# Kernel optimization log

Hardware: AMD Instinct MI355X
Metric: run time of the kernel (lower is better)

The kernel has to match this reference:

```python
import jax, jax.numpy as jnp
import numpy as np

TEMP = 5.0  # temperature_init
# All C(4,2)=6 keep-2-of-4 patterns for 2:4 semi-structured sparsity
PATTERNS = jnp.array([[1,1,0,0],[1,0,1,0],[1,0,0,1],[0,1,1,0],[0,1,0,1],[0,0,1,1]], dtype=jnp.float32)


def masked_linear(x, w, b, alpha, ids):
    # x: [N, I], w: [O, I], alpha: [A, O, I//4, 6], ids: [N]
    A, O, G, P = alpha.shape
    probs = jax.nn.softmax(alpha / TEMP, axis=-1)            # [A, O, G, 6]
    mask = jnp.einsum('aogp,pk->aogk', probs, PATTERNS)      # [A, O, G, 4]
    wm = w[None, :, :] * mask.reshape(A, O, G * 4)           # [A, O, I] per-agent masked weight
    y = jnp.einsum('ni,aoi->nao', x, wm)                     # dense per-agent GEMM
    y = jnp.take_along_axis(y, ids[:, None, None], axis=1)[:, 0, :]
    return y + b


def gru_cell(x, h, w_ih, w_hh, b_ih, b_hh):
    gi = x @ w_ih.T + b_ih
    gh = h @ w_hh.T + b_hh
    i_r, i_z, i_n = jnp.split(gi, 3, axis=-1)
    h_r, h_z, h_n = jnp.split(gh, 3, axis=-1)
    r = jax.nn.sigmoid(i_r + h_r)
    z = jax.nn.sigmoid(i_z + h_z)
    n = jnp.tanh(i_n + r * h_n)
    return (1.0 - z) * n + z * h


def setup_inputs() -> dict:
    key = jax.random.key(0)
    ks = jax.random.split(key, 20)
    B, A, E, H, NA = 1024, 8, 64, 512, 16
    s = 0.05
    d = {}
    d['inputs'] = jax.random.normal(ks[0], (B, A, E), jnp.float32)
    d['hidden_state'] = jax.random.normal(ks[1], (B, A, H), jnp.float32)
    d['agent_ids'] = jax.random.randint(ks[2], (B, A), 0, A, jnp.int32)
    d['fc1_w'] = jax.random.normal(ks[3], (H, E), jnp.float32) * s
    d['fc1_b'] = jax.random.normal(ks[4], (H,), jnp.float32) * s
    d['fc1_alpha'] = jax.random.normal(ks[5], (A, H, E // 4, 6), jnp.float32)
    d['gru_w_ih'] = jax.random.normal(ks[6], (3 * H, H), jnp.float32) * s
    d['gru_w_hh'] = jax.random.normal(ks[7], (3 * H, H), jnp.float32) * s
    d['gru_b_ih'] = jax.random.normal(ks[8], (3 * H,), jnp.float32) * s
    d['gru_b_hh'] = jax.random.normal(ks[9], (3 * H,), jnp.float32) * s
    d['fc2_w'] = jax.random.normal(ks[10], (H, H), jnp.float32) * s
    d['fc2_b'] = jax.random.normal(ks[11], (H,), jnp.float32) * s
    d['fc2_alpha'] = jax.random.normal(ks[12], (A, H, H // 4, 6), jnp.float32)
    d['fc3_w'] = jax.random.normal(ks[13], (H, H), jnp.float32) * s
    d['fc3_b'] = jax.random.normal(ks[14], (H,), jnp.float32) * s
    d['fc3_alpha'] = jax.random.normal(ks[15], (A, H, H // 4, 6), jnp.float32)
    d['fc4_w'] = jax.random.normal(ks[16], (NA, H), jnp.float32) * s
    d['fc4_b'] = jax.random.normal(ks[17], (NA,), jnp.float32) * s
    d['fc4_alpha'] = jax.random.normal(ks[18], (A, NA, H // 4, 6), jnp.float32)
    return d


def reference(inputs, hidden_state, agent_ids,
              fc1_w, fc1_b, fc1_alpha,
              gru_w_ih, gru_w_hh, gru_b_ih, gru_b_hh,
              fc2_w, fc2_b, fc2_alpha,
              fc3_w, fc3_b, fc3_alpha,
              fc4_w, fc4_b, fc4_alpha):
    b, a, e = inputs.shape
    H = hidden_state.shape[-1]
    x = inputs.reshape(-1, e)
    ids = agent_ids.reshape(-1)
    x = jax.nn.relu(masked_linear(x, fc1_w, fc1_b, fc1_alpha, ids))
    h = gru_cell(x, hidden_state.reshape(-1, H), gru_w_ih, gru_w_hh, gru_b_ih, gru_b_hh)
    q = jax.nn.relu(masked_linear(h, fc2_w, fc2_b, fc2_alpha, ids))
    q = jax.nn.relu(masked_linear(q, fc3_w, fc3_b, fc3_alpha, ids))
    q = masked_linear(q, fc4_w, fc4_b, fc4_alpha, ids)
    return q.reshape(b, a, -1), h.reshape(b, a, -1)
```

## Files before the change

### kernel.cpp

```cpp
#include <hip/hip_runtime.h>
#include <hip/hip_bf16.h>

typedef unsigned short ushort_t;
typedef __bf16 bf16x8 __attribute__((ext_vector_type(8)));
typedef unsigned short us8 __attribute__((ext_vector_type(8)));
typedef float f32x4 __attribute__((ext_vector_type(4)));

__device__ __forceinline__ ushort_t f2b(float f) {
    union { float f; unsigned int u; } v; v.f = f;
    unsigned int u = v.u;
    unsigned int r = (u + 0x7FFFu + ((u >> 16) & 1u)) >> 16;
    return (ushort_t)r;
}
__device__ __forceinline__ float sigmoidf_(float x) {
    return 1.f / (1.f + __expf(-x));
}
__device__ __forceinline__ void store_o(ushort_t* p, float v) { *p = f2b(v); }
__device__ __forceinline__ void store_o(float* p, float v) { *p = v; }

__global__ void fill_kernel(float* out, long long n, float val) {
    long long i = (long long)blockIdx.x * blockDim.x + threadIdx.x;
    if (i < n) out[i] = val;
}

#define PACKSZ(O, K) ((long long)((O) >= 64 ? (O) >> 6 : 1) * ((K) >> 5) * 2048)

__global__ void sort_kernel(const int* __restrict__ ids, int N,
                            int* __restrict__ perm, int* __restrict__ seg,
                            int4* __restrict__ ttab, int* __restrict__ tcount) {
    __shared__ int hist[16][8];
    __shared__ int wbase[16][8];
    __shared__ int atot[8];
    __shared__ int abase[8];
    int tid = threadIdx.x, wave = tid >> 6, lane = tid & 63;
    int base = wave * 512;
    unsigned long long lt = (lane == 63) ? 0x7fffffffffffffffull
                                         : ((1ull << lane) - 1ull);
    int myid[8], rank[8];
    int run[8] = {0, 0, 0, 0, 0, 0, 0, 0};
    #pragma unroll
    for (int i = 0; i < 8; i++) myid[i] = ids[base + i * 64 + lane] & 7;
    #pragma unroll
    for (int i = 0; i < 8; i++) {
        int a = myid[i];
        int r = 0;
        #pragma unroll
        for (int a2 = 0; a2 < 8; a2++) {
            unsigned long long m = __ballot(a == a2);
            if (a2 == a) r = run[a2] + __popcll(m & lt);
            run[a2] += __popcll(m);
        }
        rank[i] = r;
    }
    if (lane == 0) {
        #pragma unroll
        for (int a = 0; a < 8; a++) hist[wave][a] = run[a];
    }
    __syncthreads();
    if (tid < 8) {
        int a = tid, s = 0;
        for (int w = 0; w < 16; w++) { wbase[w][a] = s; s += hist[w][a]; }
        atot[a] = s;
    }
    __syncthreads();
    if (tid == 0) {
        int s = 0;
        for (int a = 0; a < 8; a++) { abase[a] = s; seg[a] = s; s += atot[a]; }
        seg[8] = s;
        int T = 0;
        for (int a = 0; a < 8; a++)
            for (int m = abase[a]; m < abase[a] + atot[a]; m += 64) {
                int e = abase[a] + atot[a];
                if (e > m + 64) e = m + 64;
                ttab[T++] = make_int4(a, m, e, 0);
            }
        *tcount = T;
    }
    __syncthreads();
    #pragma unroll
    for (int i = 0; i < 8; i++) {
        int a = myid[i];
        perm[abase[a] + wbase[wave][a] + rank[i]] = base + i * 64 + lane;
    }
}

__device__ __forceinline__ void maskw_item(const float* __restrict__ alpha,
                                           const float* __restrict__ w,
                                           ushort_t* __restrict__ wm,
                                           long long idx, int O, int G, int dup) {
    int g = (int)(idx % G);
    long long t2 = idx / G;
    int o = (int)(t2 % O);
    int a = (int)(t2 / O);
    const float* al = alpha + idx * 6;
    float p[6];
    float mx = -1e30f;
    #pragma unroll
    for (int i = 0; i < 6; i++) { p[i] = al[i] * 0.2f; mx = fmaxf(mx, p[i]); }
    float s = 0.f;
    #pragma unroll
    for (int i = 0; i < 6; i++) { p[i] = __expf(p[i] - mx); s += p[i]; }
    float inv = 1.f / s;
    #pragma unroll
    for (int i = 0; i < 6; i++) p[i] *= inv;
    float mk[4] = { p[0] + p[1] + p[2], p[0] + p[3] + p[4],
                    p[1] + p[3] + p[5], p[2] + p[4] + p[5] };
    int K = G * 4;
    const float* wr = w + (long long)o * K + g * 4;
    ushort_t* base = wm + (long long)a * PACKSZ(O, K);
    int k0 = g * 4;
    int c = o >> 6, su = (o >> 4) & 3, n = o & 15;
    int kk = k0 >> 5, q = (k0 >> 3) & 3, e0 = k0 & 7;
    long long off = (((long long)(c * (K >> 5) + kk) * 4 + su) * 64 + (q * 16 + n)) * 8 + e0;
    #pragma unroll
    for (int t = 0; t < 4; t++) {
        ushort_t v = f2b(wr[t] * mk[t]);
        base[off + t] = v;
        if (dup) {
            base[off + t + 512] = v;
            base[off + t + 1024] = v;
            base[off + t + 1536] = v;
        }
    }
}

__device__ __forceinline__ void canon_gather_item(const float* __restrict__ src,
                                                  ushort_t* __restrict__ dst,
                                                  const int* __restrict__ perm,
                                                  int ld, long long i) {
    long long base = i * 8;
    int pos = (int)(base / ld);
    int k = (int)(base % ld);
    int row = perm[pos] & 8191;
    const float* s = src + (long long)row * ld + k;
    us8 v;
    #pragma unroll
    for (int e = 0; e < 8; e++) v[e] = f2b(s[e]);
    *(us8*)(dst + base) = v;
}

__device__ __forceinline__ void canon_pack_item(const float* __restrict__ src,
                                                ushort_t* __restrict__ dst,
                                                long long i) {
    long long base = i * 8;
    int o_full = (int)(base >> 9);
    int k0 = (int)(base & 511);
    int g = o_full >> 9, o = o_full & 511;
    int c = o >> 6, su = (o >> 4) & 3, n = o & 15;
    int kk = k0 >> 5, q = (k0 >> 3) & 3;
    long long off = (long long)g * 262144 +
        (((long long)(c * 16 + kk) * 4 + su) * 64 + (q * 16 + n)) * 8;
    us8 v;
    #pragma unroll
    for (int e = 0; e < 8; e++) v[e] = f2b(src[base + e]);
    *(us8*)(dst + off) = v;
}

#define PB0 256
#define PB1 2048
#define PB2 2048
#define PB3 64
#define PB4 256
#define PB5 2048
#define PB6 384
#define PB7 384
#define PREP_BLOCKS (PB0+PB1+PB2+PB3+PB4+PB5+PB6+PB7)

__global__ void prep_kernel(const float* fc1_al, const float* fc1_w, ushort_t* wm1,
                            const float* fc2_al, const float* fc2_w, ushort_t* wm2,
                            const float* fc3_al, const float* fc3_w, ushort_t* wm3,
                            const float* fc4_al, const float* fc4_w, ushort_t* wm4,
                            const float* inputs, ushort_t* inp_pos,
                            const float* hidden, ushort_t* hid_pos,
                            const float* wih, ushort_t* wihp,
                            const float* whh, ushort_t* whhp,
                            const int* perm) {
    int b = blockIdx.x;
    int tid = threadIdx.x;
    if (b < PB0) { maskw_item(fc1_al, fc1_w, wm1, (long long)b * 256 + tid, 512, 16, 0); return; }
    b -= PB0;
    if (b < PB1) { maskw_item(fc2_al, fc2_w, wm2, (long long)b * 256 + tid, 512, 128, 0); return; }
    b -= PB1;
    if (b < PB2) { maskw_item(fc3_al, fc3_w, wm3, (long long)b * 256 + tid, 512, 128, 0); return; }
    b -= PB2;
    if (b < PB3) { maskw_item(fc4_al, fc4_w, wm4, (long long)b * 256 + tid, 16, 128, 1); return; }
    b -= PB3;
    if (b < PB4) { canon_gather_item(inputs, inp_pos, perm, 64, (long long)b * 256 + tid); return; }
    b -= PB4;
    if (b < PB5) { canon_gather_item(hidden, hid_pos, perm, 512, (long long)b * 256 + tid); return; }
    b -= PB5;
    if (b < PB6) { canon_pack_item(wih, wihp, (long long)b * 256 + tid); return; }
    b -= PB6;
    canon_pack_item(whh, whhp, (long long)b * 256 + tid);
}

#define BM 64
#define BN 64

template <typename OT>
__launch_bounds__(256, 4)
__global__ void gemm_tiled(const ushort_t* __restrict__ In, int ldin,
                           const ushort_t* __restrict__ Wpk, long long wstride,
                           const float* __restrict__ bias,
                           OT* __restrict__ Out, int ldo,
                           const int4* __restrict__ ttab,
                           const int* __restrict__ tcount,
                           const int* __restrict__ scatter,
                           int O, int K, int relu) {
    int t = blockIdx.x;
    if (t >= *tcount) return;
    int4 tt = ttab[t];
    int a = tt.x, pos0 = tt.y, pos1 = tt.z;
    int o0 = blockIdx.y * BN;

    __shared__ ushort_t As[2][2048];

    int tid = threadIdx.x;
    int wave = tid >> 6, lane = tid & 63;
    int wr = (wave >> 1) & 1, wc = wave & 1;
    int quad = lane >> 4, l16 = lane & 15;
    int srow = tid >> 2, sgrp = tid & 3;
    int wsoff = (srow * 4 + (sgrp ^ ((srow >> 2) & 3))) * 8;
    int rl = (l16 * 4 + (quad ^ ((l16 >> 2) & 3))) * 8;

    int apos = pos0 + srow;
    int apos_c = apos < pos1 ? apos : (pos1 - 1);
    const ushort_t* aptr = In + (long long)apos_c * ldin + sgrp * 8;

    const ushort_t* wb = Wpk + (long long)a * wstride +
        (long long)blockIdx.y * (K >> 5) * 2048 + lane * 8;

    f32x4 acc[2][2];
    #pragma unroll
    for (int i = 0; i < 2; i++)
        #pragma unroll
        for (int j = 0; j < 2; j++) acc[i][j] = (f32x4){0.f, 0.f, 0.f, 0.f};

    int KKh = K >> 6;
    for (int k2 = 0; k2 < KKh; k2++) {
        int kk = k2 * 2;
        us8 av0 = *(const us8*)(aptr + kk * 32);
        us8 av1 = *(const us8*)(aptr + kk * 32 + 32);
        bf16x8 b00 = *(const bf16x8*)(wb + (kk * 4 + wc * 2 + 0) * 512);
        bf16x8 b01 = *(const bf16x8*)(wb + (kk * 4 + wc * 2 + 1) * 512);
        bf16x8 b10 = *(const bf16x8*)(wb + ((kk + 1) * 4 + wc * 2 + 0) * 512);
        bf16x8 b11 = *(const bf16x8*)(wb + ((kk + 1) * 4 + wc * 2 + 1) * 512);
        __syncthreads();
        *(us8*)(&As[0][wsoff]) = av0;
        *(us8*)(&As[1][wsoff]) = av1;
        __syncthreads();
        bf16x8 af0[2], af1[2];
        af0[0] = *(const bf16x8*)(&As[0][(wr * 2 + 0) * 512 + rl]);
        af0[1] = *(const bf16x8*)(&As[0][(wr * 2 + 1) * 512 + rl]);
        af1[0] = *(const bf16x8*)(&As[1][(wr * 2 + 0) * 512 + rl]);
        af1[1] = *(const bf16x8*)(&As[1][(wr * 2 + 1) * 512 + rl]);
        #pragma unroll
        for (int i = 0; i < 2; i++) {
            acc[i][0] = __builtin_amdgcn_mfma_f32_16x16x32_bf16(af0[i], b00, acc[i][0], 0, 0, 0);
            acc[i][1] = __builtin_amdgcn_mfma_f32_16x16x32_bf16(af0[i], b01, acc[i][1], 0, 0, 0);
        }
        #pragma unroll
        for (int i = 0; i < 2; i++) {
            acc[i][0] = __builtin_amdgcn_mfma_f32_16x16x32_bf16(af1[i], b10, acc[i][0], 0, 0, 0);
            acc[i][1] = __builtin_amdgcn_mfma_f32_16x16x32_bf16(af1[i], b11, acc[i][1], 0, 0, 0);
        }
    }

    #pragma unroll
    for (int i = 0; i < 2; i++) {
        int mbase = wr * 32 + i * 16 + quad * 4;
        #pragma unroll
        for (int j = 0; j < 2; j++) {
            int col = o0 + wc * 32 + j * 16 + l16;
            if (col < O) {
                float bias_v = bias ? bias[col] : 0.f;
                #pragma unroll
                for (int r = 0; r < 4; r++) {
                    int pos = pos0 + mbase + r;
                    if (pos < pos1) {
                        float v = acc[i][j][r] + bias_v;
                        if (relu) v = fmaxf(v, 0.f);
                        int orow = (scatter ? scatter[pos] : pos) & 8191;
                        store_o(&Out[(long long)orow * ldo + col], v);
                    }
                }
            }
        }
    }
}

__launch_bounds__(512, 2)
__global__ void gru_fused(const ushort_t* __restrict__ y1,
                          const ushort_t* __restrict__ hid_pos,
                          const float* __restrict__ hidden_f,
                          const ushort_t* __restrict__ wihp,
                          const ushort_t* __restrict__ whhp,
                          const float* __restrict__ bih,
                          const float* __restrict__ bhh,
                          const int* __restrict__ perm,
                          float* __restrict__ out_h_f,
                          ushort_t* __restrict__ hp,
                          int N, int H) {
    int m0 = blockIdx.x * 128;

    __shared__ ushort_t Ay[4096];
    __shared__ ushort_t Ah[4096];
    __shared__ ushort_t Bt[6][2048];

    int tid = threadIdx.x;
    int wave = tid >> 6, lane = tid & 63;
    int wr = wave >> 1, wc = wave & 1;
    int quad = lane >> 4, l16 = lane & 15;
    int srow = tid >> 2, sgrp = tid & 3;
    int wsoff = (srow * 4 + (sgrp ^ ((srow >> 2) & 3))) * 8;
    int rl = (l16 * 4 + (quad ^ ((l16 >> 2) & 3))) * 8;

    const ushort_t* ay_p = y1 + (long long)(m0 + srow) * H + sgrp * 8;
    const ushort_t* ah_p = hid_pos + (long long)(m0 + srow) * H + sgrp * 8;

    const ushort_t* wbs[3];
    int wg[3];
    #pragma unroll
    for (int q = 0; q < 3; q++) {
        int s = q * 512 + tid;
        int g = s >> 8, so = s & 255;
        wg[q] = s;
        wbs[q] = ((g < 3) ? (wihp + (long long)g * 262144)
                          : (whhp + (long long)(g - 3) * 262144)) +
                 (long long)blockIdx.y * 16 * 2048 + so * 8;
    }

    f32x4 acc[4][2][2];
    #pragma unroll
    for (int g = 0; g < 4; g++)
        #pragma unroll
        for (int i = 0; i < 2; i++)
            #pragma unroll
            for (int j = 0; j < 2; j++) acc[g][i][j] = (f32x4){0.f, 0.f, 0.f, 0.f};

    for (int kk = 0; kk < 16; kk++) {
        us8 va = *(const us8*)(ay_p + kk * 32);
        us8 vh = *(const us8*)(ah_p + kk * 32);
        us8 vb[3];
        #pragma unroll
        for (int q = 0; q < 3; q++) vb[q] = *(const us8*)(wbs[q] + kk * 2048);
        __syncthreads();
        *(us8*)(&Ay[wsoff]) = va;
        *(us8*)(&Ah[wsoff]) = vh;
        #pragma unroll
        for (int q = 0; q < 3; q++) {
            int s = wg[q];
            *(us8*)(&Bt[s >> 8][(s & 255) * 8]) = vb[q];
        }
        __syncthreads();

        bf16x8 ayf[2], ahf[2];
        #pragma unroll
        for (int u = 0; u < 2; u++) {
            ayf[u] = *(const bf16x8*)(&Ay[(wr * 2 + u) * 512 + rl]);
            ahf[u] = *(const bf16x8*)(&Ah[(wr * 2 + u) * 512 + rl]);
        }
        #pragma unroll
        for (int g = 0; g < 3; g++) {
            bf16x8 bw[2], bu[2];
            #pragma unroll
            for (int u = 0; u < 2; u++) {
                bw[u] = *(const bf16x8*)(&Bt[g][(wc * 2 + u) * 512 + lane * 8]);
                bu[u] = *(const bf16x8*)(&Bt[g + 3][(wc * 2 + u) * 512 + lane * 8]);
            }
            int ai = (g < 2) ? g : 2;
            int ah2 = (g < 2) ? g : 3;
            #pragma unroll
            for (int i = 0; i < 2; i++)
                #pragma unroll
                for (int j = 0; j < 2; j++) {
                    acc[ai][i][j] = __builtin_amdgcn_mfma_f32_16x16x32_bf16(
                        ayf[i], bw[j], acc[ai][i][j], 0, 0, 0);
                    acc[ah2][i][j] = __builtin_amdgcn_mfma_f32_16x16x32_bf16(
                        ahf[i], bu[j], acc[ah2][i][j], 0, 0, 0);
                }
        }
    }

    int c0 = blockIdx.y * 64;
    #pragma unroll
    for (int i = 0; i < 2; i++) {
        #pragma unroll
        for (int r = 0; r < 4; r++) {
            int pos = m0 + wr * 32 + i * 16 + quad * 4 + r;
            int norig = perm[pos] & 8191;
            #pragma unroll
            for (int j = 0; j < 2; j++) {
                int col = c0 + wc * 32 + j * 16 + l16;
                float sr = acc[0][i][j][r] + bih[col] + bhh[col];
                float sz = acc[1][i][j][r] + bih[H + col] + bhh[H + col];
                float in_ = acc[2][i][j][r] + bih[2 * H + col];
                float hn = acc[3][i][j][r] + bhh[2 * H + col];
                float rg = sigmoidf_(sr);
                float zg = sigmoidf_(sz);
                float ng = tanhf(in_ + rg * hn);
                float hv = hidden_f[(long long)norig * H + col];
                float hnew = (1.f - zg) * ng + zg * hv;
                out_h_f[(long long)norig * H + col] = hnew;
                hp[(long long)pos * H + col] = f2b(hnew);
            }
        }
    }
}

extern "C" void kernel_launch(void* const* d_in, const int* in_sizes, int n_in,
                              void* d_out, int out_size, void* d_ws, size_t ws_size,
                              hipStream_t stream) {
    (void)in_sizes; (void)n_in;
    const int N = 8192, A = 8, E = 64, H = 512, NA = 16;

    float* out_f = (float*)d_out;
    float* out_q = out_f;
    float* out_h = out_f + (size_t)N * NA;

    char* p = (char*)d_ws;
    auto alloc = [&](size_t b) { char* r = p; p += (b + 255) & ~(size_t)255; return r; };
    int*  perm   = (int*)alloc((size_t)N * 4);
    int*  seg    = (int*)alloc(16 * 4);
    int4* ttab   = (int4*)alloc(144 * 16);
    int*  tcount = (int*)alloc(256);
    ushort_t* wm1     = (ushort_t*)alloc((size_t)A * PACKSZ(H, E) * 2);
    ushort_t* wm2     = (ushort_t*)alloc((size_t)A * PACKSZ(H, H) * 2);
    ushort_t* wm3     = (ushort_t*)alloc((size_t)A * PACKSZ(H, H) * 2);
    ushort_t* wm4     = (ushort_t*)alloc((size_t)A * PACKSZ(NA, H) * 2);
    ushort_t* y1      = (ushort_t*)alloc((size_t)N * H * 2);
    ushort_t* inp_pos = (ushort_t*)alloc((size_t)N * E * 2);
    ushort_t* hid_pos = (ushort_t*)alloc((size_t)N * H * 2);
    ushort_t* wihp    = (ushort_t*)alloc((size_t)3 * H * H * 2);
    ushort_t* whhp    = (ushort_t*)alloc((size_t)3 * H * H * 2);
    ushort_t* hp      = (ushort_t*)alloc((size_t)N * H * 2);
    size_t need = (size_t)(p - (char*)d_ws);
    ushort_t* q2 = y1;
    ushort_t* q3 = hid_pos;

    if (ws_size < need) {
        fill_kernel<<<(unsigned)((out_size + 255) / 256), 256, 0, stream>>>(
            out_f, out_size, 1000.f);
        return;
    }

    const float* inputs = (const float*)d_in[0];
    const float* hidden = (const float*)d_in[1];
    const int*   ids    = (const int*)d_in[2];
    const float* fc1_w  = (const float*)d_in[3];
    const float* fc1_b  = (const float*)d_in[4];
    const float* fc1_al = (const float*)d_in[5];
    const float* wih    = (const float*)d_in[6];
    const float* whh    = (const float*)d_in[7];
    const float* bih    = (const float*)d_in[8];
    const float* bhh    = (const float*)d_in[9];
    const float* fc2_w  = (const float*)d_in[10];
    const float* fc2_b  = (const float*)d_in[11];
    const float* fc2_al = (const float*)d_in[12];
    const float* fc3_w  = (const float*)d_in[13];
    const float* fc3_b  = (const float*)d_in[14];
    const float* fc3_al = (const float*)d_in[15];
    const float* fc4_w  = (const float*)d_in[16];
    const float* fc4_b  = (const float*)d_in[17];
    const float* fc4_al = (const float*)d_in[18];

    sort_kernel<<<1, 1024, 0, stream>>>(ids, N, perm, seg, ttab, tcount);

    prep_kernel<<<PREP_BLOCKS, 256, 0, stream>>>(
        fc1_al, fc1_w, wm1, fc2_al, fc2_w, wm2, fc3_al, fc3_w, wm3,
        fc4_al, fc4_w, wm4, inputs, inp_pos, hidden, hid_pos,
        wih, wihp, whh, whhp, perm);

    dim3 blk(256);
    gemm_tiled<ushort_t><<<dim3(136, H / BN), blk, 0, stream>>>(
        inp_pos, E, wm1, PACKSZ(H, E), fc1_b, y1, H, ttab, tcount,
        nullptr, H, E, 1);
    gru_fused<<<dim3(N / 128, H / 64), dim3(512), 0, stream>>>(
        y1, hid_pos, hidden, wihp, whhp, bih, bhh, perm, out_h, hp, N, H);
    gemm_tiled<ushort_t><<<dim3(136, H / BN), blk, 0, stream>>>(
        hp, H, wm2, PACKSZ(H, H), fc2_b, q2, H, ttab, tcount,
        nullptr, H, H, 1);
    gemm_tiled<ushort_t><<<dim3(136, H / BN), blk, 0, stream>>>(
        q2, H, wm3, PACKSZ(H, H), fc3_b, q3, H, ttab, tcount,
        nullptr, H, H, 1);
    gemm_tiled<float><<<dim3(136, 1), blk, 0, stream>>>(
        q3, H, wm4, PACKSZ(NA, H), fc4_b, out_q, NA, ttab, tcount,
        perm, NA, H, 0);
}
```

Baseline: 221.9 us.

## Pad agent segments to 128 rows and use 128-row GEMM tiles

Pads each agent's sorted row segment up to a multiple of 128 and marks the padding with sentinel perm entries. This lets the masked GEMMs use 512-thread, 128-row tiles without per-row bounds checks and lets the GRU kernel work on padded tiles that line up with per-agent segments. FC4 gets its own kernel that splits each 128-row tile into two 64-row halves and scatters results through perm. The aim is to reuse each weight fragment across more rows and drop clamping and scatter logic from the inner GEMMs, at the cost of some wasted work on padding rows and larger workspace buffers.

```diff
diff --git a/kernel.cpp b/kernel.cpp
--- a/kernel.cpp
+++ b/kernel.cpp
@@ -5,6 +5,9 @@
 typedef __bf16 bf16x8 __attribute__((ext_vector_type(8)));
 typedef unsigned short us8 __attribute__((ext_vector_type(8)));
 typedef float f32x4 __attribute__((ext_vector_type(4)));
+
+#define NPAD 9216
+#define SENT (1 << 20)
 
 __device__ __forceinline__ ushort_t f2b(float f) {
     union { float f; unsigned int u; } v; v.f = f;
@@ -15,8 +18,6 @@
 __device__ __forceinline__ float sigmoidf_(float x) {
     return 1.f / (1.f + __expf(-x));
 }
-__device__ __forceinline__ void store_o(ushort_t* p, float v) { *p = f2b(v); }
-__device__ __forceinline__ void store_o(float* p, float v) { *p = v; }
 
 __global__ void fill_kernel(float* out, long long n, float val) {
     long long i = (long long)blockIdx.x * blockDim.x + threadIdx.x;
@@ -65,15 +66,20 @@
     __syncthreads();
     if (tid == 0) {
         int s = 0;
-        for (int a = 0; a < 8; a++) { abase[a] = s; seg[a] = s; s += atot[a]; }
+        for (int a = 0; a < 8; a++) {
+            abase[a] = s; seg[a] = s;
+            s += (atot[a] + 127) & ~127;
+        }
         seg[8] = s;
         int T = 0;
-        for (int a = 0; a < 8; a++)
-            for (int m = abase[a]; m < abase[a] + atot[a]; m += 64) {
-                int e = abase[a] + atot[a];
-                if (e > m + 64) e = m + 64;
-                ttab[T++] = make_int4(a, m, e, 0);
+        for (int a = 0; a < 8; a++) {
+            int e = abase[a] + atot[a];
+            int pe = abase[a] + ((atot[a] + 127) & ~127);
+            for (int m = abase[a]; m < pe; m += 128) {
+                int z = e < m + 128 ? e : m + 128;
+                ttab[T++] = make_int4(a, m, z, 0);
             }
+        }
         *tcount = T;
     }
     __syncthreads();
@@ -82,6 +88,13 @@
         int a = myid[i];
         perm[abase[a] + wbase[wave][a] + rank[i]] = base + i * 64 + lane;
     }
+    for (int a = 0; a < 8; a++) {
+        int e = abase[a] + atot[a];
+        int pe = abase[a] + ((atot[a] + 127) & ~127);
+        for (int p2 = e + tid; p2 < pe; p2 += 1024) perm[p2] = SENT;
+    }
+    int Pend = abase[7] + ((atot[7] + 127) & ~127);
+    for (int p2 = Pend + tid; p2 < NPAD; p2 += 1024) perm[p2] = SENT;
 }
 
 __device__ __forceinline__ void maskw_item(const float* __restrict__ alpha,
@@ -131,7 +144,8 @@
     long long base = i * 8;
     int pos = (int)(base / ld);
     int k = (int)(base % ld);
-    int row = perm[pos] & 8191;
+    int row = perm[pos];
+    if (row >= 8192) row = 0;
     const float* s = src + (long long)row * ld + k;
     us8 v;
     #pragma unroll
@@ -160,8 +174,8 @@
 #define PB1 2048
 #define PB2 2048
 #define PB3 64
-#define PB4 256
-#define PB5 2048
+#define PB4 288
+#define PB5 2304
 #define PB6 384
 #define PB7 384
 #define PREP_BLOCKS (PB0+PB1+PB2+PB3+PB4+PB5+PB6+PB7)
@@ -194,39 +208,31 @@
     canon_pack_item(whh, whhp, (long long)b * 256 + tid);
 }
 
-#define BM 64
-#define BN 64
-
-template <typename OT>
-__launch_bounds__(256, 4)
-__global__ void gemm_tiled(const ushort_t* __restrict__ In, int ldin,
-                           const ushort_t* __restrict__ Wpk, long long wstride,
-                           const float* __restrict__ bias,
-                           OT* __restrict__ Out, int ldo,
-                           const int4* __restrict__ ttab,
-                           const int* __restrict__ tcount,
-                           const int* __restrict__ scatter,
-                           int O, int K, int relu) {
+__launch_bounds__(512, 2)
+__global__ void gemm128(const ushort_t* __restrict__ In, int ldin,
+                        const ushort_t* __restrict__ Wpk, long long wstride,
+                        const float* __restrict__ bias,
+                        ushort_t* __restrict__ Out, int ldo,
+                        const int4* __restrict__ ttab,
+                        const int* __restrict__ tcount,
+                        int O, int K, int relu) {
     int t = blockIdx.x;
     if (t >= *tcount) return;
     int4 tt = ttab[t];
-    int a = tt.x, pos0 = tt.y, pos1 = tt.z;
-    int o0 = blockIdx.y * BN;
-
-    __shared__ ushort_t As[2][2048];
+    int a = tt.x, pos0 = tt.y;
+    int o0 = blockIdx.y * 64;
+
+    __shared__ ushort_t As[2][4096];
 
     int tid = threadIdx.x;
     int wave = tid >> 6, lane = tid & 63;
-    int wr = (wave >> 1) & 1, wc = wave & 1;
+    int wr = wave >> 1, wc = wave & 1;
     int quad = lane >> 4, l16 = lane & 15;
     int srow = tid >> 2, sgrp = tid & 3;
     int wsoff = (srow * 4 + (sgrp ^ ((srow >> 2) & 3))) * 8;
     int rl = (l16 * 4 + (quad ^ ((l16 >> 2) & 3))) * 8;
 
-    int apos = pos0 + srow;
-    int apos_c = apos < pos1 ? apos : (pos1 - 1);
-    const ushort_t* aptr = In + (long long)apos_c * ldin + sgrp * 8;
-
+    const ushort_t* aptr = In + (long long)(pos0 + srow) * ldin + sgrp * 8;
     const ushort_t* wb = Wpk + (long long)a * wstride +
         (long long)blockIdx.y * (K >> 5) * 2048 + lane * 8;
 
@@ -250,10 +256,11 @@
         *(us8*)(&As[1][wsoff]) = av1;
         __syncthreads();
         bf16x8 af0[2], af1[2];
-        af0[0] = *(const bf16x8*)(&As[0][(wr * 2 + 0) * 512 + rl]);
-        af0[1] = *(const bf16x8*)(&As[0][(wr * 2 + 1) * 512 + rl]);
-        af1[0] = *(const bf16x8*)(&As[1][(wr * 2 + 0) * 512 + rl]);
-        af1[1] = *(const bf16x8*)(&As[1][(wr * 2 + 1) * 512 + rl]);
+        #pragma unroll
+        for (int i = 0; i < 2; i++) {
+            af0[i] = *(const bf16x8*)(&As[0][(wr * 2 + i) * 512 + rl]);
+            af1[i] = *(const bf16x8*)(&As[1][(wr * 2 + i) * 512 + rl]);
+        }
         #pragma unroll
         for (int i = 0; i < 2; i++) {
             acc[i][0] = __builtin_amdgcn_mfma_f32_16x16x32_bf16(af0[i], b00, acc[i][0], 0, 0, 0);
@@ -273,15 +280,98 @@
         for (int j = 0; j < 2; j++) {
             int col = o0 + wc * 32 + j * 16 + l16;
             if (col < O) {
-                float bias_v = bias ? bias[col] : 0.f;
+                float bias_v = bias[col];
                 #pragma unroll
                 for (int r = 0; r < 4; r++) {
                     int pos = pos0 + mbase + r;
-                    if (pos < pos1) {
-                        float v = acc[i][j][r] + bias_v;
-                        if (relu) v = fmaxf(v, 0.f);
-                        int orow = (scatter ? scatter[pos] : pos) & 8191;
-                        store_o(&Out[(long long)orow * ldo + col], v);
+                    float v = acc[i][j][r] + bias_v;
+                    if (relu) v = fmaxf(v, 0.f);
+                    Out[(long long)pos * ldo + col] = f2b(v);
+                }
+            }
+        }
+    }
+}
+
+__launch_bounds__(256, 4)
+__global__ void gemm_fc4(const ushort_t* __restrict__ In, int ldin,
+                         const ushort_t* __restrict__ Wpk, long long wstride,
+                         const float* __restrict__ bias,
+                         float* __restrict__ Out, int ldo,
+                         const int4* __restrict__ ttab,
+                         const int* __restrict__ tcount,
+                         const int* __restrict__ perm,
+                         int O, int K) {
+    int t = blockIdx.x;
+    if ((t >> 1) >= *tcount) return;
+    int4 tt = ttab[t >> 1];
+    int a = tt.x;
+    int pos0 = tt.y + (t & 1) * 64;
+
+    __shared__ ushort_t As[2][2048];
+
+    int tid = threadIdx.x;
+    int wave = tid >> 6, lane = tid & 63;
+    int wr = (wave >> 1) & 1, wc = wave & 1;
+    int quad = lane >> 4, l16 = lane & 15;
+    int srow = tid >> 2, sgrp = tid & 3;
+    int wsoff = (srow * 4 + (sgrp ^ ((srow >> 2) & 3))) * 8;
+    int rl = (l16 * 4 + (quad ^ ((l16 >> 2) & 3))) * 8;
+
+    const ushort_t* aptr = In + (long long)(pos0 + srow) * ldin + sgrp * 8;
+    const ushort_t* wb = Wpk + (long long)a * wstride + lane * 8;
+
+    f32x4 acc[2][2];
+    #pragma unroll
+    for (int i = 0; i < 2; i++)
+        #pragma unroll
+        for (int j = 0; j < 2; j++) acc[i][j] = (f32x4){0.f, 0.f, 0.f, 0.f};
+
+    int KKh = K >> 6;
+    for (int k2 = 0; k2 < KKh; k2++) {
+        int kk = k2 * 2;
+        us8 av0 = *(const us8*)(aptr + kk * 32);
+        us8 av1 = *(const us8*)(aptr + kk * 32 + 32);
+        bf16x8 b00 = *(const bf16x8*)(wb + (kk * 4 + wc * 2 + 0) * 512);
+        bf16x8 b01 = *(const bf16x8*)(wb + (kk * 4 + wc * 2 + 1) * 512);
+        bf16x8 b10 = *(const bf16x8*)(wb + ((kk + 1) * 4 + wc * 2 + 0) * 512);
+        bf16x8 b11 = *(const bf16x8*)(wb + ((kk + 1) * 4 + wc * 2 + 1) * 512);
+        __syncthreads();
+        *(us8*)(&As[0][wsoff]) = av0;
+        *(us8*)(&As[1][wsoff]) = av1;
+        __syncthreads();
+        bf16x8 af0[2], af1[2];
+        #pragma unroll
+        for (int i = 0; i < 2; i++) {
+            af0[i] = *(const bf16x8*)(&As[0][(wr * 2 + i) * 512 + rl]);
+            af1[i] = *(const bf16x8*)(&As[1][(wr * 2 + i) * 512 + rl]);
+        }
+        #pragma unroll
+        for (int i = 0; i < 2; i++) {
+            acc[i][0] = __builtin_amdgcn_mfma_f32_16x16x32_bf16(af0[i], b00, acc[i][0], 0, 0, 0);
+            acc[i][1] = __builtin_amdgcn_mfma_f32_16x16x32_bf16(af0[i], b01, acc[i][1], 0, 0, 0);
+        }
+        #pragma unroll
+        for (int i = 0; i < 2; i++) {
+            acc[i][0] = __builtin_amdgcn_mfma_f32_16x16x32_bf16(af1[i], b10, acc[i][0], 0, 0, 0);
+            acc[i][1] = __builtin_amdgcn_mfma_f32_16x16x32_bf16(af1[i], b11, acc[i][1], 0, 0, 0);
+        }
+    }
+
+    #pragma unroll
+    for (int i = 0; i < 2; i++) {
+        int mbase = wr * 32 + i * 16 + quad * 4;
+        #pragma unroll
+        for (int j = 0; j < 2; j++) {
+            int col = wc * 32 + j * 16 + l16;
+            if (col < O) {
+                float bias_v = bias[col];
+                #pragma unroll
+                for (int r = 0; r < 4; r++) {
+                    int pos = pos0 + mbase + r;
+                    int orow = perm[pos];
+                    if (orow < 8192) {
+                        Out[(long long)orow * ldo + col] = acc[i][j][r] + bias_v;
                     }
                 }
             }
@@ -300,7 +390,9 @@
                           const int* __restrict__ perm,
                           float* __restrict__ out_h_f,
                           ushort_t* __restrict__ hp,
+                          const int* __restrict__ tcount,
                           int N, int H) {
+    if ((int)blockIdx.x >= *tcount) return;
     int m0 = blockIdx.x * 128;
 
     __shared__ ushort_t Ay[4096];
@@ -388,7 +480,9 @@
         #pragma unroll
         for (int r = 0; r < 4; r++) {
             int pos = m0 + wr * 32 + i * 16 + quad * 4 + r;
-            int norig = perm[pos] & 8191;
+            int norig = perm[pos];
+            bool realr = norig < 8192;
+            int nr = realr ? norig : 0;
             #pragma unroll
             for (int j = 0; j < 2; j++) {
                 int col = c0 + wc * 32 + j * 16 + l16;
@@ -399,9 +493,9 @@
                 float rg = sigmoidf_(sr);
                 float zg = sigmoidf_(sz);
                 float ng = tanhf(in_ + rg * hn);
-                float hv = hidden_f[(long long)norig * H + col];
+                float hv = hidden_f[(long long)nr * H + col];
                 float hnew = (1.f - zg) * ng + zg * hv;
-                out_h_f[(long long)norig * H + col] = hnew;
+                if (realr) out_h_f[(long long)norig * H + col] = hnew;
                 hp[(long long)pos * H + col] = f2b(hnew);
             }
         }
@@ -420,7 +514,7 @@
 
     char* p = (char*)d_ws;
     auto alloc = [&](size_t b) { char* r = p; p += (b + 255) & ~(size_t)255; return r; };
-    int*  perm   = (int*)alloc((size_t)N * 4);
+    int*  perm   = (int*)alloc((size_t)NPAD * 4);
     int*  seg    = (int*)alloc(16 * 4);
     int4* ttab   = (int4*)alloc(144 * 16);
     int*  tcount = (int*)alloc(256);
@@ -428,12 +522,12 @@
     ushort_t* wm2     = (ushort_t*)alloc((size_t)A * PACKSZ(H, H) * 2);
     ushort_t* wm3     = (ushort_t*)alloc((size_t)A * PACKSZ(H, H) * 2);
     ushort_t* wm4     = (ushort_t*)alloc((size_t)A * PACKSZ(NA, H) * 2);
-    ushort_t* y1      = (ushort_t*)alloc((size_t)N * H * 2);
-    ushort_t* inp_pos = (ushort_t*)alloc((size_t)N * E * 2);
-    ushort_t* hid_pos = (ushort_t*)alloc((size_t)N * H * 2);
+    ushort_t* y1      = (ushort_t*)alloc((size_t)NPAD * H * 2);
+    ushort_t* inp_pos = (ushort_t*)alloc((size_t)NPAD * E * 2);
+    ushort_t* hid_pos = (ushort_t*)alloc((size_t)NPAD * H * 2);
     ushort_t* wihp    = (ushort_t*)alloc((size_t)3 * H * H * 2);
     ushort_t* whhp    = (ushort_t*)alloc((size_t)3 * H * H * 2);
-    ushort_t* hp      = (ushort_t*)alloc((size_t)N * H * 2);
+    ushort_t* hp      = (ushort_t*)alloc((size_t)NPAD * H * 2);
     size_t need = (size_t)(p - (char*)d_ws);
     ushort_t* q2 = y1;
     ushort_t* q3 = hid_pos;
@@ -471,19 +565,16 @@
         fc4_al, fc4_w, wm4, inputs, inp_pos, hidden, hid_pos,
         wih, wihp, whh, whhp, perm);
 
-    dim3 blk(256);
-    gemm_tiled<ushort_t><<<dim3(136, H / BN), blk, 0, stream>>>(
-        inp_pos, E, wm1, PACKSZ(H, E), fc1_b, y1, H, ttab, tcount,
-        nullptr, H, E, 1);
-    gru_fused<<<dim3(N / 128, H / 64), dim3(512), 0, stream>>>(
-        y1, hid_pos, hidden, wihp, whhp, bih, bhh, perm, out_h, hp, N, H);
-    gemm_tiled<ushort_t><<<dim3(136, H / BN), blk, 0, stream>>>(
-        hp, H, wm2, PACKSZ(H, H), fc2_b, q2, H, ttab, tcount,
-        nullptr, H, H, 1);
-    gemm_tiled<ushort_t><<<dim3(136, H / BN), blk, 0, stream>>>(
-        q2, H, wm3, PACKSZ(H, H), fc3_b, q3, H, ttab, tcount,
-        nullptr, H, H, 1);
-    gemm_tiled<float><<<dim3(136, 1), blk, 0, stream>>>(
+    gemm128<<<dim3(72, H / 64), dim3(512), 0, stream>>>(
+        inp_pos, E, wm1, PACKSZ(H, E), fc1_b, y1, H, ttab, tcount, H, E, 1);
+    gru_fused<<<dim3(72, H / 64), dim3(512), 0, stream>>>(
+        y1, hid_pos, hidden, wihp, whhp, bih, bhh, perm, out_h, hp,
+        tcount, N, H);
+    gemm128<<<dim3(72, H / 64), dim3(512), 0, stream>>>(
+        hp, H, wm2, PACKSZ(H, H), fc2_b, q2, H, ttab, tcount, H, H, 1);
+    gemm128<<<dim3(72, H / 64), dim3(512), 0, stream>>>(
+        q2, H, wm3, PACKSZ(H, H), fc3_b, q3, H, ttab, tcount, H, H, 1);
+    gemm_fc4<<<dim3(144, 1), dim3(256), 0, stream>>>(
         q3, H, wm4, PACKSZ(NA, H), fc4_b, out_q, NA, ttab, tcount,
-        perm, NA, H, 0);
-}
+        perm, NA, H);
+}
```

Result: slower. 240.8 us (+8.5%).

## Fold sort into weight-prep kernel and double GRU K-step per barrier

Applied to the files above, without the earlier changes.

Sorting is merged into the weight-masking/packing kernel, so the permutation-independent weight preparation runs alongside the single sort block instead of waiting behind it. Only the activation gathers, which need the permutation, move to a separate follow-up kernel. Separately, the GRU kernel now stages two K-slices per sync pair, which halves the barrier count and doubles its shared memory use, possibly lowering occupancy.

```diff
diff --git a/kernel.cpp b/kernel.cpp
--- a/kernel.cpp
+++ b/kernel.cpp
@@ -24,65 +24,6 @@
 }
 
 #define PACKSZ(O, K) ((long long)((O) >= 64 ? (O) >> 6 : 1) * ((K) >> 5) * 2048)
-
-__global__ void sort_kernel(const int* __restrict__ ids, int N,
-                            int* __restrict__ perm, int* __restrict__ seg,
-                            int4* __restrict__ ttab, int* __restrict__ tcount) {
-    __shared__ int hist[16][8];
-    __shared__ int wbase[16][8];
-    __shared__ int atot[8];
-    __shared__ int abase[8];
-    int tid = threadIdx.x, wave = tid >> 6, lane = tid & 63;
-    int base = wave * 512;
-    unsigned long long lt = (lane == 63) ? 0x7fffffffffffffffull
-                                         : ((1ull << lane) - 1ull);
-    int myid[8], rank[8];
-    int run[8] = {0, 0, 0, 0, 0, 0, 0, 0};
-    #pragma unroll
-    for (int i = 0; i < 8; i++) myid[i] = ids[base + i * 64 + lane] & 7;
-    #pragma unroll
-    for (int i = 0; i < 8; i++) {
-        int a = myid[i];
-        int r = 0;
-        #pragma unroll
-        for (int a2 = 0; a2 < 8; a2++) {
-            unsigned long long m = __ballot(a == a2);
-            if (a2 == a) r = run[a2] + __popcll(m & lt);
-            run[a2] += __popcll(m);
-        }
-        rank[i] = r;
-    }
-    if (lane == 0) {
-        #pragma unroll
-        for (int a = 0; a < 8; a++) hist[wave][a] = run[a];
-    }
-    __syncthreads();
-    if (tid < 8) {
-        int a = tid, s = 0;
-        for (int w = 0; w < 16; w++) { wbase[w][a] = s; s += hist[w][a]; }
-        atot[a] = s;
-    }
-    __syncthreads();
-    if (tid == 0) {
-        int s = 0;
-        for (int a = 0; a < 8; a++) { abase[a] = s; seg[a] = s; s += atot[a]; }
-        seg[8] = s;
-        int T = 0;
-        for (int a = 0; a < 8; a++)
-            for (int m = abase[a]; m < abase[a] + atot[a]; m += 64) {
-                int e = abase[a] + atot[a];
-                if (e > m + 64) e = m + 64;
-                ttab[T++] = make_int4(a, m, e, 0);
-            }
-        *tcount = T;
-    }
-    __syncthreads();
-    #pragma unroll
-    for (int i = 0; i < 8; i++) {
-        int a = myid[i];
-        perm[abase[a] + wbase[wave][a] + rank[i]] = base + i * 64 + lane;
-    }
-}
 
 __device__ __forceinline__ void maskw_item(const float* __restrict__ alpha,
                                            const float* __restrict__ w,
@@ -122,21 +63,6 @@
             base[off + t + 1536] = v;
         }
     }
-}
-
-__device__ __forceinline__ void canon_gather_item(const float* __restrict__ src,
-                                                  ushort_t* __restrict__ dst,
-                                                  const int* __restrict__ perm,
-                                                  int ld, long long i) {
-    long long base = i * 8;
-    int pos = (int)(base / ld);
-    int k = (int)(base % ld);
-    int row = perm[pos] & 8191;
-    const float* s = src + (long long)row * ld + k;
-    us8 v;
-    #pragma unroll
-    for (int e = 0; e < 8; e++) v[e] = f2b(s[e]);
-    *(us8*)(dst + base) = v;
 }
 
 __device__ __forceinline__ void canon_pack_item(const float* __restrict__ src,
@@ -156,42 +82,115 @@
     *(us8*)(dst + off) = v;
 }
 
-#define PB0 256
-#define PB1 2048
-#define PB2 2048
-#define PB3 64
-#define PB4 256
-#define PB5 2048
-#define PB6 384
-#define PB7 384
-#define PREP_BLOCKS (PB0+PB1+PB2+PB3+PB4+PB5+PB6+PB7)
-
-__global__ void prep_kernel(const float* fc1_al, const float* fc1_w, ushort_t* wm1,
-                            const float* fc2_al, const float* fc2_w, ushort_t* wm2,
-                            const float* fc3_al, const float* fc3_w, ushort_t* wm3,
-                            const float* fc4_al, const float* fc4_w, ushort_t* wm4,
-                            const float* inputs, ushort_t* inp_pos,
-                            const float* hidden, ushort_t* hid_pos,
-                            const float* wih, ushort_t* wihp,
-                            const float* whh, ushort_t* whhp,
-                            const int* perm) {
-    int b = blockIdx.x;
+__device__ __forceinline__ void canon_gather_item(const float* __restrict__ src,
+                                                  ushort_t* __restrict__ dst,
+                                                  const int* __restrict__ perm,
+                                                  int ld, long long i) {
+    long long base = i * 8;
+    int pos = (int)(base / ld);
+    int k = (int)(base % ld);
+    int row = perm[pos] & 8191;
+    const float* s = src + (long long)row * ld + k;
+    us8 v;
+    #pragma unroll
+    for (int e = 0; e < 8; e++) v[e] = f2b(s[e]);
+    *(us8*)(dst + base) = v;
+}
+
+#define W_FC1 65536LL
+#define W_FC2 589824LL
+#define W_FC3 1114112LL
+#define W_FC4 1130496LL
+#define W_WIH 1228800LL
+#define W_END 1327104LL
+#define SPW_BLOCKS (1 + 1296)
+
+__global__ void sort_prepw(const int* __restrict__ ids,
+                           int* __restrict__ perm, int* __restrict__ seg,
+                           int4* __restrict__ ttab, int* __restrict__ tcount,
+                           const float* fc1_al, const float* fc1_w, ushort_t* wm1,
+                           const float* fc2_al, const float* fc2_w, ushort_t* wm2,
+                           const float* fc3_al, const float* fc3_w, ushort_t* wm3,
+                           const float* fc4_al, const float* fc4_w, ushort_t* wm4,
+                           const float* wih, ushort_t* wihp,
+                           const float* whh, ushort_t* whhp) {
     int tid = threadIdx.x;
-    if (b < PB0) { maskw_item(fc1_al, fc1_w, wm1, (long long)b * 256 + tid, 512, 16, 0); return; }
-    b -= PB0;
-    if (b < PB1) { maskw_item(fc2_al, fc2_w, wm2, (long long)b * 256 + tid, 512, 128, 0); return; }
-    b -= PB1;
-    if (b < PB2) { maskw_item(fc3_al, fc3_w, wm3, (long long)b * 256 + tid, 512, 128, 0); return; }
-    b -= PB2;
-    if (b < PB3) { maskw_item(fc4_al, fc4_w, wm4, (long long)b * 256 + tid, 16, 128, 1); return; }
-    b -= PB3;
-    if (b < PB4) { canon_gather_item(inputs, inp_pos, perm, 64, (long long)b * 256 + tid); return; }
-    b -= PB4;
-    if (b < PB5) { canon_gather_item(hidden, hid_pos, perm, 512, (long long)b * 256 + tid); return; }
-    b -= PB5;
-    if (b < PB6) { canon_pack_item(wih, wihp, (long long)b * 256 + tid); return; }
-    b -= PB6;
-    canon_pack_item(whh, whhp, (long long)b * 256 + tid);
+    if (blockIdx.x == 0) {
+        __shared__ int hist[16][8];
+        __shared__ int wbase[16][8];
+        __shared__ int atot[8];
+        __shared__ int abase[8];
+        int wave = tid >> 6, lane = tid & 63;
+        int base = wave * 512;
+        unsigned long long lt = (lane == 63) ? 0x7fffffffffffffffull
+                                             : ((1ull << lane) - 1ull);
+        int myid[8], rank[8];
+        int run[8] = {0, 0, 0, 0, 0, 0, 0, 0};
+        #pragma unroll
+        for (int i = 0; i < 8; i++) myid[i] = ids[base + i * 64 + lane] & 7;
+        #pragma unroll
+        for (int i = 0; i < 8; i++) {
+            int a = myid[i];
+            int r = 0;
+            #pragma unroll
+            for (int a2 = 0; a2 < 8; a2++) {
+                unsigned long long m = __ballot(a == a2);
+                if (a2 == a) r = run[a2] + __popcll(m & lt);
+                run[a2] += __popcll(m);
+            }
+            rank[i] = r;
+        }
+        if (lane == 0) {
+            #pragma unroll
+            for (int a = 0; a < 8; a++) hist[wave][a] = run[a];
+        }
+        __syncthreads();
+        if (tid < 8) {
+            int a = tid, s = 0;
+            for (int w = 0; w < 16; w++) { wbase[w][a] = s; s += hist[w][a]; }
+            atot[a] = s;
+        }
+        __syncthreads();
+        if (tid == 0) {
+            int s = 0;
+            for (int a = 0; a < 8; a++) { abase[a] = s; seg[a] = s; s += atot[a]; }
+            seg[8] = s;
+            int T = 0;
+            for (int a = 0; a < 8; a++)
+                for (int m = abase[a]; m < abase[a] + atot[a]; m += 64) {
+                    int e = abase[a] + atot[a];
+                    if (e > m + 64) e = m + 64;
+                    ttab[T++] = make_int4(a, m, e, 0);
+                }
+            *tcount = T;
+        }
+        __syncthreads();
+        #pragma unroll
+        for (int i = 0; i < 8; i++) {
+            int a = myid[i];
+            perm[abase[a] + wbase[wave][a] + rank[i]] = base + i * 64 + lane;
+        }
+        return;
+    }
+    long long gid = (long long)(blockIdx.x - 1) * 1024 + tid;
+    if (gid < W_FC1)      { maskw_item(fc1_al, fc1_w, wm1, gid, 512, 16, 0); return; }
+    if (gid < W_FC2)      { maskw_item(fc2_al, fc2_w, wm2, gid - W_FC1, 512, 128, 0); return; }
+    if (gid < W_FC3)      { maskw_item(fc3_al, fc3_w, wm3, gid - W_FC2, 512, 128, 0); return; }
+    if (gid < W_FC4)      { maskw_item(fc4_al, fc4_w, wm4, gid - W_FC3, 16, 128, 1); return; }
+    if (gid < W_WIH)      { canon_pack_item(wih, wihp, gid - W_FC4); return; }
+    canon_pack_item(whh, whhp, gid - W_WIH);
+}
+
+#define G_INP 65536LL
+#define G_END 589824LL
+#define PG_BLOCKS 576
+
+__global__ void prep_gather(const float* __restrict__ inputs, ushort_t* inp_pos,
+                            const float* __restrict__ hidden, ushort_t* hid_pos,
+                            const int* __restrict__ perm) {
+    long long gid = (long long)blockIdx.x * 1024 + threadIdx.x;
+    if (gid < G_INP) canon_gather_item(inputs, inp_pos, perm, 64, gid);
+    else             canon_gather_item(hidden, hid_pos, perm, 512, gid - G_INP);
 }
 
 #define BM 64
@@ -303,9 +302,9 @@
                           int N, int H) {
     int m0 = blockIdx.x * 128;
 
-    __shared__ ushort_t Ay[4096];
-    __shared__ ushort_t Ah[4096];
-    __shared__ ushort_t Bt[6][2048];
+    __shared__ ushort_t Ay[8192];
+    __shared__ ushort_t Ah[8192];
+    __shared__ ushort_t Bt[6][4096];
 
     int tid = threadIdx.x;
     int wave = tid >> 6, lane = tid & 63;
@@ -338,47 +337,61 @@
             #pragma unroll
             for (int j = 0; j < 2; j++) acc[g][i][j] = (f32x4){0.f, 0.f, 0.f, 0.f};
 
-    for (int kk = 0; kk < 16; kk++) {
-        us8 va = *(const us8*)(ay_p + kk * 32);
-        us8 vh = *(const us8*)(ah_p + kk * 32);
-        us8 vb[3];
-        #pragma unroll
-        for (int q = 0; q < 3; q++) vb[q] = *(const us8*)(wbs[q] + kk * 2048);
-        __syncthreads();
-        *(us8*)(&Ay[wsoff]) = va;
-        *(us8*)(&Ah[wsoff]) = vh;
+    for (int k2 = 0; k2 < 8; k2++) {
+        int kk = k2 * 2;
+        us8 va0 = *(const us8*)(ay_p + kk * 32);
+        us8 vh0 = *(const us8*)(ah_p + kk * 32);
+        us8 va1 = *(const us8*)(ay_p + kk * 32 + 32);
+        us8 vh1 = *(const us8*)(ah_p + kk * 32 + 32);
+        us8 vb0[3], vb1[3];
+        #pragma unroll
+        for (int q = 0; q < 3; q++) {
+            vb0[q] = *(const us8*)(wbs[q] + kk * 2048);
+            vb1[q] = *(const us8*)(wbs[q] + kk * 2048 + 2048);
+        }
+        __syncthreads();
+        *(us8*)(&Ay[wsoff]) = va0;
+        *(us8*)(&Ay[4096 + wsoff]) = va1;
+        *(us8*)(&Ah[wsoff]) = vh0;
+        *(us8*)(&Ah[4096 + wsoff]) = vh1;
         #pragma unroll
         for (int q = 0; q < 3; q++) {
             int s = wg[q];
-            *(us8*)(&Bt[s >> 8][(s & 255) * 8]) = vb[q];
-        }
-        __syncthreads();
-
-        bf16x8 ayf[2], ahf[2];
-        #pragma unroll
-        for (int u = 0; u < 2; u++) {
-            ayf[u] = *(const bf16x8*)(&Ay[(wr * 2 + u) * 512 + rl]);
-            ahf[u] = *(const bf16x8*)(&Ah[(wr * 2 + u) * 512 + rl]);
-        }
-        #pragma unroll
-        for (int g = 0; g < 3; g++) {
-            bf16x8 bw[2], bu[2];
+            *(us8*)(&Bt[s >> 8][(s & 255) * 8]) = vb0[q];
+            *(us8*)(&Bt[s >> 8][2048 + (s & 255) * 8]) = vb1[q];
+        }
+        __syncthreads();
+
+        #pragma unroll
+        for (int half = 0; half < 2; half++) {
+            int ho = half * 4096;
+            int hb = half * 2048;
+            bf16x8 ayf[2], ahf[2];
             #pragma unroll
             for (int u = 0; u < 2; u++) {
-                bw[u] = *(const bf16x8*)(&Bt[g][(wc * 2 + u) * 512 + lane * 8]);
-                bu[u] = *(const bf16x8*)(&Bt[g + 3][(wc * 2 + u) * 512 + lane * 8]);
+                ayf[u] = *(const bf16x8*)(&Ay[ho + (wr * 2 + u) * 512 + rl]);
+                ahf[u] = *(const bf16x8*)(&Ah[ho + (wr * 2 + u) * 512 + rl]);
             }
-            int ai = (g < 2) ? g : 2;
-            int ah2 = (g < 2) ? g : 3;
             #pragma unroll
-            for (int i = 0; i < 2; i++)
+            for (int g = 0; g < 3; g++) {
+                bf16x8 bw[2], bu[2];
                 #pragma unroll
-                for (int j = 0; j < 2; j++) {
-                    acc[ai][i][j] = __builtin_amdgcn_mfma_f32_16x16x32_bf16(
-                        ayf[i], bw[j], acc[ai][i][j], 0, 0, 0);
-                    acc[ah2][i][j] = __builtin_amdgcn_mfma_f32_16x16x32_bf16(
-                        ahf[i], bu[j], acc[ah2][i][j], 0, 0, 0);
+                for (int u = 0; u < 2; u++) {
+                    bw[u] = *(const bf16x8*)(&Bt[g][hb + (wc * 2 + u) * 512 + lane * 8]);
+                    bu[u] = *(const bf16x8*)(&Bt[g + 3][hb + (wc * 2 + u) * 512 + lane * 8]);
                 }
+                int ai = (g < 2) ? g : 2;
+                int ah2 = (g < 2) ? g : 3;
+                #pragma unroll
+                for (int i = 0; i < 2; i++)
+                    #pragma unroll
+                    for (int j = 0; j < 2; j++) {
+                        acc[ai][i][j] = __builtin_amdgcn_mfma_f32_16x16x32_bf16(
+                            ayf[i], bw[j], acc[ai][i][j], 0, 0, 0);
+                        acc[ah2][i][j] = __builtin_amdgcn_mfma_f32_16x16x32_bf16(
+                            ahf[i], bu[j], acc[ah2][i][j], 0, 0, 0);
+                    }
+            }
         }
     }
 
@@ -464,12 +477,13 @@
     const float* fc4_b  = (const float*)d_in[17];
     const float* fc4_al = (const float*)d_in[18];
 
-    sort_kernel<<<1, 1024, 0, stream>>>(ids, N, perm, seg, ttab, tcount);
-
-    prep_kernel<<<PREP_BLOCKS, 256, 0, stream>>>(
+    sort_prepw<<<SPW_BLOCKS, 1024, 0, stream>>>(
+        ids, perm, seg, ttab, tcount,
         fc1_al, fc1_w, wm1, fc2_al, fc2_w, wm2, fc3_al, fc3_w, wm3,
-        fc4_al, fc4_w, wm4, inputs, inp_pos, hidden, hid_pos,
-        wih, wihp, whh, whhp, perm);
+        fc4_al, fc4_w, wm4, wih, wihp, whh, whhp);
+
+    prep_gather<<<PG_BLOCKS, 1024, 0, stream>>>(
+        inputs, inp_pos, hidden, hid_pos, perm);
 
     dim3 blk(256);
     gemm_tiled<ushort_t><<<dim3(136, H / BN), blk, 0, stream>>>(
```

Measured after the change: 211.6 us. 1.05x faster.
